# Performance work log

Hardware: AMD Instinct MI355X
Metric: run time of the kernel (lower is better)

## Reference

```python
import jax, jax.numpy as jnp
import numpy as np

OUT = 7          # output_size
SR = 2           # sampling_ratio
SCALE = 1.0 / 16.0  # 1 / feature_stride


def _context_boxes(boxes):
    """8 surrounding cells of a 3x3 grid around each RoI; offset-major concat ([8N,4])."""
    x1, y1, x2, y2 = boxes[:, 0], boxes[:, 1], boxes[:, 2], boxes[:, 3]
    w = (x2 - x1) / 3.0
    h = (y2 - y1) / 3.0
    offs = []
    for i in range(3):
        for j in range(3):
            if i == 1 and j == 1:
                continue
            dx = j * w
            dy = i * h
            offs.append(jnp.stack([x1 + dx, y1 + dy, x1 + dx + w, y1 + dy + h], axis=1))
    return jnp.concatenate(offs, axis=0)


def _roi_align_v2(feat, boxes, scale, out, sr):
    """ROIAlignV2 (aligned=True). feat [C,H,W], boxes [B,4] xyxy -> [B,C,out,out]."""
    C, H, W = feat.shape
    # aligned: half-pixel offset, no max(roi_size, 1)
    x1 = boxes[:, 0] * scale - 0.5
    y1 = boxes[:, 1] * scale - 0.5
    bw = (boxes[:, 2] * scale - 0.5 - x1) / out   # bin width
    bh = (boxes[:, 3] * scale - 0.5 - y1) / out   # bin height
    # sample positions along each axis: start + (bin + (s+0.5)/sr) * bin_size  -> [B, out*sr]
    g = jnp.arange(out * sr) // sr
    s = jnp.arange(out * sr) % sr
    t = g + (s + 0.5) / sr                         # [out*sr]
    ys = y1[:, None] + t[None, :] * bh[:, None]    # [B,S]
    xs = x1[:, None] + t[None, :] * bw[:, None]    # [B,S]

    def axis(p, size):
        valid = (p >= -1.0) & (p <= size)
        p = jnp.clip(p, 0.0, size - 1.0)
        lo = jnp.clip(jnp.floor(p), 0.0, size - 2.0).astype(jnp.int32)
        return lo, p - lo, valid

    yl, fy, vy = axis(ys, H)
    xl, fx, vx = axis(xs, W)
    Y = yl[:, :, None]          # [B,S,1]
    X = xl[:, None, :]          # [B,1,S]
    f00 = feat[:, Y, X]         # [C,B,S,S]
    f01 = feat[:, Y, X + 1]
    f10 = feat[:, Y + 1, X]
    f11 = feat[:, Y + 1, X + 1]
    wy = fy[:, :, None]
    wx = fx[:, None, :]
    v = (f00 * (1 - wy) * (1 - wx) + f01 * (1 - wy) * wx
         + f10 * wy * (1 - wx) + f11 * wy * wx)
    v = v * (vy[:, :, None] & vx[:, None, :]).astype(v.dtype)
    # average the sr x sr samples inside each output bin
    B = boxes.shape[0]
    v = v.reshape(C, B, out, sr, out, sr).mean(axis=(3, 5))
    return v.transpose(1, 0, 2, 3)  # [B,C,out,out]


def setup_inputs() -> dict:
    key = jax.random.key(0)
    k1, k2, k3, k4 = jax.random.split(key, 4)
    features = jax.random.normal(k1, (256, 64, 64), dtype=jnp.float32)  # stride-16 map of a 1024px image
    N = 128
    xy = jax.random.uniform(k2, (N, 2), minval=0.0, maxval=800.0)
    wh = jax.random.uniform(k3, (N, 2), minval=32.0, maxval=220.0)
    boxes = jnp.concatenate([xy, xy + wh], axis=1)                      # [N,4] xyxy, image coords
    w_fuse = jax.random.normal(k4, (256, 2048), dtype=jnp.float32) * 0.02  # Conv2d(2048,256,1) weight
    b_fuse = jnp.zeros((256,), dtype=jnp.float32)
    return {"features": features, "boxes": boxes, "w_fuse": w_fuse, "b_fuse": b_fuse}


def reference(features, boxes, w_fuse, b_fuse):
    N = boxes.shape[0]
    cboxes = _context_boxes(boxes)                               # [8N,4] offset-major
    pooled = _roi_align_v2(features, cboxes, SCALE, OUT, SR)     # [8N,256,7,7]
    chunk = pooled.reshape(N, -1, OUT, OUT)                      # faithful to torch .view(N,-1,7,7)
    out = jnp.einsum('nchw,oc->nohw', chunk, w_fuse) + b_fuse[None, :, None, None]
    return jax.nn.relu(out)                                      # [N,256,7,7]
```

## Files before the change

kernel.cpp:

```cpp
#include <hip/hip_runtime.h>
#include <hip/hip_fp16.h>

#define SCALE (1.0f/16.0f)

typedef __attribute__((ext_vector_type(8))) _Float16 f16x8;
typedef __attribute__((ext_vector_type(4))) float f32x4;
typedef __attribute__((ext_vector_type(16))) float f32x16;
typedef __attribute__((ext_vector_type(4))) unsigned int u32x4;
typedef unsigned int u32;

__device__ __forceinline__ void gload16(const void* g, void* l) {
    __builtin_amdgcn_global_load_lds(
        (const __attribute__((address_space(1))) unsigned int*)g,
        (__attribute__((address_space(3))) unsigned int*)l, 16, 0, 0);
}
__device__ __forceinline__ __half2 asH2(u32 v) {
    union { u32 i; __half2 h; } u; u.i = v; return u.h;
}
__device__ __forceinline__ u32 asU32(__half2 h) {
    union { __half2 h; u32 i; } u; u.h = h; return u.i;
}
__device__ __forceinline__ int dupH2(float f) {
    __half h = __float2half_rn(f);
    __half2 d; d.x = h; d.y = h;
    union { __half2 h2; int i; } u; u.h2 = d; return u.i;
}

__global__ void k_prep(const float* __restrict__ feat, __half* __restrict__ featT,
                       const float* __restrict__ wf, __half* __restrict__ wr) {
    __shared__ float t[64][65];
    int b = blockIdx.x;
    if (b < 256) {
        int cb = (b >> 6) << 6;
        int pb = (b & 63) << 6;
        int lx = threadIdx.x & 63, ly = threadIdx.x >> 6;
#pragma unroll
        for (int i = 0; i < 16; ++i) {
            int cl = i*4 + ly;
            t[cl][lx] = feat[(size_t)(cb + cl) * 4096 + pb + lx];
        }
        __syncthreads();
#pragma unroll
        for (int i = 0; i < 16; ++i) {
            int pl = i*4 + ly;
            featT[(size_t)(pb + pl) * 256 + cb + lx] = __float2half_rn(t[lx][pl]);
        }
    } else {
        int ch = (b - 256) * 256 + threadIdx.x;
        int l  = ch & 63;
        int sk = (ch >> 6) & 15;
        int ot = (ch >> 10) & 7;
        int j  = ch >> 13;
        int o = ot*32 + (l & 31);
        int k = j*256 + sk*16 + (l >> 5)*8;
        const float* src = wf + (size_t)o*2048 + k;
        f32x4 a = *(const f32x4*)src;
        f32x4 bb = *(const f32x4*)(src + 4);
        f16x8 p;
#pragma unroll
        for (int u = 0; u < 4; ++u) p[u] = (_Float16)a[u];
#pragma unroll
        for (int u = 0; u < 4; ++u) p[4+u] = (_Float16)bb[u];
        *((f16x8*)wr + ch) = p;
    }
}

__global__ void __launch_bounds__(512, 2) k_fused(
    const __half* __restrict__ featT,
    const float* __restrict__ boxes,
    const __half* __restrict__ wr,
    const float* __restrict__ bfuse,
    float* __restrict__ out)
{
    __shared__ char patch[2][32768];
    __shared__ char Pl[2][16384];
    __shared__ int4 tabs[4][2][7];
    __shared__ int  pbs[4][2];

    int tid = threadIdx.x;
    int lane = tid & 63, wid = tid >> 6;
    int r31 = lane & 31, l5 = lane >> 5;
    int bid = blockIdx.x;
    int n  = bid & 127;
    int hh = bid >> 7;
    int HWn = hh ? 17 : 32;

    int nb_base = (n & 15) * 8;
    int off = n >> 4;
    int t3 = off + (off >= 4 ? 1 : 0);
    int ci = t3 / 3, cj = t3 - ci*3;

    f32x16 acc;
#pragma unroll
    for (int i = 0; i < 16; ++i) acc[i] = 0.f;

    auto tablesW = [&](int jj, int isy, bool active) {
        if (active) {
            int nbx = nb_base + jj;
            float bx1 = boxes[nbx*4+0], by1 = boxes[nbx*4+1];
            float bx2 = boxes[nbx*4+2], by2 = boxes[nbx*4+3];
            float w3 = (bx2-bx1)*(1.f/3.f), h3 = (by2-by1)*(1.f/3.f);
            float org  = isy ? (by1 + ci*h3)*SCALE - 0.5f : (bx1 + cj*w3)*SCALE - 0.5f;
            float step = (isy ? h3 : w3) * (SCALE*(1.f/14.f));
            float sc = isy ? 0.25f : 1.f;
            float p = org + ((float)lane + 0.5f)*step;
            float pc = fminf(fmaxf(p, 0.f), 63.f);
            float fl = fminf(floorf(pc), 62.f);
            float fr = pc - fl;
            float c0 = __shfl(fl, 2*lane);
            float c1 = __shfl(fl, 2*lane+1);
            float f  = __shfl(fr, 2*lane);
            float f2 = __shfl(fr, 2*lane+1);
            float fl0 = __shfl(fl, 0);
            int base = min((int)fl0, 56);
            float d = c1 - c0;
            float a0 = sc*((1.f-f) + (1.f-d)*(1.f-f2));
            float a1 = sc*(f + (1.f-d)*f2 + d*(1.f-f2));
            float a2 = sc*(d*f2);
            if (lane < 7) {
                int4 e;
                e.x = (int)c0 - base;
                e.y = dupH2(a0); e.z = dupH2(a1); e.w = dupH2(a2);
                tabs[jj & 3][isy][lane] = e;
            }
            if (lane == 0) pbs[jj & 3][isy] = base;
        }
    };

    auto patchStage = [&](int jj) {
        int xb = pbs[jj & 3][0], yb = pbs[jj & 3][1];
        const __half* src = featT + ((size_t)((yb + wid)*64 + xb))*256 + lane*8;
        char* dst = patch[jj & 1] + wid*4096;
#pragma unroll
        for (int seg = 0; seg < 4; ++seg)
            gload16(src + seg*512, dst + seg*1024);
    };

    auto pool = [&](int jj) {
        int buf = jj & 1;
        int co = tid & 31;
        int e0 = tid >> 5;
        const char* pb = patch[buf] + co*16;
        for (int e = e0; e < HWn; e += 16) {
            int g = hh*32 + e;
            int h = (g*37) >> 8, w = g - h*7;
            int4 tx = tabs[jj & 3][0][w], ty = tabs[jj & 3][1][h];
            int px0 = tx.x, py0 = ty.x;
            int lx2 = min(px0 + 2, 7), ly2 = min(py0 + 2, 7);
            const char* r0 = pb + (py0*8 + px0)*512;
            const char* r1 = pb + (min(py0+1,7)*8 + px0)*512;
            const char* r2 = pb + (ly2*8 + px0)*512;
            int dx2 = (lx2 - px0)*512;
            u32x4 F00 = *(const u32x4*)(r0);
            u32x4 F01 = *(const u32x4*)(r0 + 512);
            u32x4 F02 = *(const u32x4*)(r0 + dx2);
            u32x4 F10 = *(const u32x4*)(r1);
            u32x4 F11 = *(const u32x4*)(r1 + 512);
            u32x4 F12 = *(const u32x4*)(r1 + dx2);
            u32x4 F20 = *(const u32x4*)(r2);
            u32x4 F21 = *(const u32x4*)(r2 + 512);
            u32x4 F22 = *(const u32x4*)(r2 + dx2);
            __half2 xa = asH2(tx.y), xb2 = asH2(tx.z), xc = asH2(tx.w);
            __half2 ya = asH2(ty.y), yb2 = asH2(ty.z), yc = asH2(ty.w);
            u32x4 res;
#pragma unroll
            for (int s = 0; s < 4; ++s) {
                __half2 q0 = __hfma2(asH2(F02[s]), xc, __hfma2(asH2(F01[s]), xb2, __hmul2(asH2(F00[s]), xa)));
                __half2 q1 = __hfma2(asH2(F12[s]), xc, __hfma2(asH2(F11[s]), xb2, __hmul2(asH2(F10[s]), xa)));
                __half2 q2 = __hfma2(asH2(F22[s]), xc, __hfma2(asH2(F21[s]), xb2, __hmul2(asH2(F20[s]), xa)));
                res[s] = asU32(__hfma2(q2, yc, __hfma2(q1, yb2, __hmul2(q0, ya))));
            }
            *(u32x4*)(Pl[buf] + e*512 + ((co*16) ^ ((e & 7) << 4))) = res;
        }
    };

    f16x8 Wf[2][16];
    auto prefW = [&](int j) {
        const f16x8* wb = (const f16x8*)wr + (size_t)((j*8 + wid)*16)*64 + lane;
#pragma unroll
        for (int sk = 0; sk < 16; ++sk) Wf[j & 1][sk] = wb[sk*64];
    };

    auto gemm = [&](int j) {
        int buf = j & 1;
#pragma unroll
        for (int sk = 0; sk < 16; ++sk) {
            int byo = r31*512 + ((sk*32 + l5*16) ^ ((r31 & 7) << 4));
            f16x8 pf = *(const f16x8*)(Pl[buf] + byo);
            acc = __builtin_amdgcn_mfma_f32_32x32x16_f16(Wf[j & 1][sk], pf, acc, 0, 0, 0);
        }
    };

    tablesW(wid >> 1, wid & 1, wid < 6);
    __syncthreads();
    prefW(0);
    patchStage(0);
    patchStage(1);
    __syncthreads();
    pool(0);
    __syncthreads();

#pragma unroll
    for (int j = 0; j < 8; ++j) {
        if (j < 7) prefW(j+1);
        if (j < 6) patchStage(j+2);
        gemm(j);
        if (j < 7) pool(j+1);
        if (j < 5) tablesW(j+3, wid, wid < 2);
        __syncthreads();
    }

    int hw = hh*32 + r31;
    if (hw < 49) {
        float* ob = out + (size_t)n*12544 + hw;
#pragma unroll
        for (int reg = 0; reg < 16; ++reg) {
            int o = wid*32 + (reg & 3) + 8*(reg >> 2) + 4*l5;
            float v = acc[reg] + bfuse[o];
            ob[(size_t)o*49] = fmaxf(v, 0.f);
        }
    }
}

extern "C" void kernel_launch(void* const* d_in, const int* in_sizes, int n_in,
                              void* d_out, int out_size, void* d_ws, size_t ws_size,
                              hipStream_t stream) {
    const float* feat  = (const float*)d_in[0];
    const float* boxes = (const float*)d_in[1];
    const float* wf    = (const float*)d_in[2];
    const float* bfuse = (const float*)d_in[3];
    float* out = (float*)d_out;

    char* ws = (char*)d_ws;
    __half* wr    = (__half*)ws;
    __half* featT = (__half*)(ws + (1u<<20));

    k_prep<<<512, 256, 0, stream>>>(feat, featT, wf, wr);
    k_fused<<<256, 512, 0, stream>>>(featT, boxes, wr, bfuse, out);
}
```

Before: 30.91 us.

## Split GEMM K across wave pairs with two output tiles per wave

Each wave now computes two 32-wide output-channel tiles over half of the K dimension, so every pooled LDS fragment feeds two MFMAs and pooled-tile LDS reads are halved. The partial sums are combined through LDS in a final reduction step before bias and ReLU. Weight prefetch uses explicit ping-pong register arrays pinned with empty asm to keep the loads in flight, and the occupancy hint in the launch bounds is dropped. This costs a second accumulator, an extra barrier with reduction traffic, and higher register pressure that may lower occupancy.

Result: no change. 31.00 us (+0.3%).

```diff
diff --git a/kernel.cpp b/kernel.cpp
--- a/kernel.cpp
+++ b/kernel.cpp
@@ -8,6 +8,10 @@
 typedef __attribute__((ext_vector_type(16))) float f32x16;
 typedef __attribute__((ext_vector_type(4))) unsigned int u32x4;
 typedef unsigned int u32;
+
+#define PIN16(W) { _Pragma("unroll") \
+    for (int s_ = 0; s_ < 16; ++s_) \
+        asm volatile("" : "+v"((W)[s_][0]), "+v"((W)[s_][1]), "+v"((W)[s_][2]), "+v"((W)[s_][3])); }
 
 __device__ __forceinline__ void gload16(const void* g, void* l) {
     __builtin_amdgcn_global_load_lds(
@@ -65,7 +69,7 @@
     }
 }
 
-__global__ void __launch_bounds__(512, 2) k_fused(
+__global__ void __launch_bounds__(512) k_fused(
     const __half* __restrict__ featT,
     const float* __restrict__ boxes,
     const __half* __restrict__ wr,
@@ -80,6 +84,7 @@
     int tid = threadIdx.x;
     int lane = tid & 63, wid = tid >> 6;
     int r31 = lane & 31, l5 = lane >> 5;
+    int oq = wid & 3, kh = wid >> 2;
     int bid = blockIdx.x;
     int n  = bid & 127;
     int hh = bid >> 7;
@@ -90,9 +95,9 @@
     int t3 = off + (off >= 4 ? 1 : 0);
     int ci = t3 / 3, cj = t3 - ci*3;
 
-    f32x16 acc;
-#pragma unroll
-    for (int i = 0; i < 16; ++i) acc[i] = 0.f;
+    f32x16 acc0, acc1;
+#pragma unroll
+    for (int i = 0; i < 16; ++i) { acc0[i] = 0.f; acc1[i] = 0.f; }
 
     auto tablesW = [&](int jj, int isy, bool active) {
         if (active) {
@@ -174,50 +179,91 @@
         }
     };
 
-    f16x8 Wf[2][16];
-    auto prefW = [&](int j) {
-        const f16x8* wb = (const f16x8*)wr + (size_t)((j*8 + wid)*16)*64 + lane;
-#pragma unroll
-        for (int sk = 0; sk < 16; ++sk) Wf[j & 1][sk] = wb[sk*64];
-    };
-
-    auto gemm = [&](int j) {
-        int buf = j & 1;
-#pragma unroll
-        for (int sk = 0; sk < 16; ++sk) {
+    u32x4 WfA[16], WfB[16];
+    auto prefW = [&](u32x4* dst, int j) {
+#pragma unroll
+        for (int t = 0; t < 2; ++t) {
+            int ot = oq*2 + t;
+            const u32x4* wb = (const u32x4*)wr + ((size_t)((j*8 + ot)*16 + kh*8))*64 + lane;
+#pragma unroll
+            for (int s = 0; s < 8; ++s) dst[t*8 + s] = wb[s*64];
+        }
+    };
+
+    auto gemm = [&](const u32x4* Wsrc, int j) {
+        const char* plb = (j & 1) ? Pl[1] : Pl[0];
+        f16x8 pf[8];
+#pragma unroll
+        for (int s = 0; s < 8; ++s) {
+            int sk = kh*8 + s;
             int byo = r31*512 + ((sk*32 + l5*16) ^ ((r31 & 7) << 4));
-            f16x8 pf = *(const f16x8*)(Pl[buf] + byo);
-            acc = __builtin_amdgcn_mfma_f32_32x32x16_f16(Wf[j & 1][sk], pf, acc, 0, 0, 0);
+            pf[s] = *(const f16x8*)(plb + byo);
+        }
+#pragma unroll
+        for (int s = 0; s < 8; ++s) {
+            acc0 = __builtin_amdgcn_mfma_f32_32x32x16_f16(
+                __builtin_bit_cast(f16x8, Wsrc[s]), pf[s], acc0, 0, 0, 0);
+            acc1 = __builtin_amdgcn_mfma_f32_32x32x16_f16(
+                __builtin_bit_cast(f16x8, Wsrc[8 + s]), pf[s], acc1, 0, 0, 0);
         }
     };
 
     tablesW(wid >> 1, wid & 1, wid < 6);
     __syncthreads();
-    prefW(0);
+    prefW(WfA, 0);
     patchStage(0);
     patchStage(1);
+    PIN16(WfA);
     __syncthreads();
     pool(0);
     __syncthreads();
 
 #pragma unroll
     for (int j = 0; j < 8; ++j) {
-        if (j < 7) prefW(j+1);
+        if (j < 7) prefW((j & 1) ? WfA : WfB, j+1);
         if (j < 6) patchStage(j+2);
-        gemm(j);
+        gemm((j & 1) ? WfB : WfA, j);
         if (j < 7) pool(j+1);
         if (j < 5) tablesW(j+3, wid, wid < 2);
+        if (j < 7) { if (j & 1) { PIN16(WfA); } else { PIN16(WfB); } }
         __syncthreads();
     }
 
-    int hw = hh*32 + r31;
-    if (hw < 49) {
+    float* red = (float*)&patch[0][0];
+    if (kh == 1) {
+#pragma unroll
+        for (int t = 0; t < 2; ++t) {
+            f32x16 a = t ? acc1 : acc0;
+#pragma unroll
+            for (int q = 0; q < 4; ++q) {
+                f32x4 v;
+#pragma unroll
+                for (int i = 0; i < 4; ++i) v[i] = a[q*4 + i];
+                int byo = (oq*2 + t)*4096 + r31*128 + ((q*32 + l5*16) ^ ((r31 & 7) << 4));
+                *(f32x4*)((char*)red + byo) = v;
+            }
+        }
+    }
+    __syncthreads();
+    if (kh == 0) {
+        int hw = hh*32 + r31;
+        bool ok = hw < 49;
         float* ob = out + (size_t)n*12544 + hw;
 #pragma unroll
-        for (int reg = 0; reg < 16; ++reg) {
-            int o = wid*32 + (reg & 3) + 8*(reg >> 2) + 4*l5;
-            float v = acc[reg] + bfuse[o];
-            ob[(size_t)o*49] = fmaxf(v, 0.f);
+        for (int t = 0; t < 2; ++t) {
+            f32x16 a = t ? acc1 : acc0;
+            int otb = (oq*2 + t)*32;
+#pragma unroll
+            for (int q = 0; q < 4; ++q) {
+                int byo = (oq*2 + t)*4096 + r31*128 + ((q*32 + l5*16) ^ ((r31 & 7) << 4));
+                f32x4 r = *(const f32x4*)((const char*)red + byo);
+#pragma unroll
+                for (int i = 0; i < 4; ++i) {
+                    int o = otb + q*8 + l5*4 + i;
+                    float v = a[q*4 + i] + r[i] + bfuse[o];
+                    if (ok) ob[(size_t)o*49] = fmaxf(v, 0.f);
+                }
+            }
         }
     }
 }
```
